# Kernel tuning notes

Hardware: AMD Instinct MI355X
Metric: run time of the kernel (lower is better)

The kernel has to match this reference:

```python
import jax, jax.numpy as jnp
import numpy as np

INPUT_DIM = 128
HIDDEN_DIM = 512
STACK_DIM = 64
BATCH = 128
MAX_T = 259  # 2*128 + 3
SEQ_L = 259  # l, so k = (l-3)//2 = 128


def setup_inputs() -> dict:
    key = jax.random.key(0)
    ks = jax.random.split(key, 7)
    G = 4 * HIDDEN_DIM
    x = jax.random.normal(ks[0], (SEQ_L, BATCH, INPUT_DIM), dtype=jnp.float32)
    Wih = jax.random.normal(ks[1], (G, INPUT_DIM + STACK_DIM), dtype=jnp.float32) * 0.05
    bih = jax.random.normal(ks[2], (G,), dtype=jnp.float32) * 0.05
    Whh = jax.random.normal(ks[3], (G, HIDDEN_DIM), dtype=jnp.float32) * 0.05
    bhh = jax.random.normal(ks[4], (G,), dtype=jnp.float32) * 0.05
    Wr = jax.random.normal(ks[5], (INPUT_DIM + STACK_DIM + 2, HIDDEN_DIM), dtype=jnp.float32) * 0.05
    br = jax.random.normal(ks[6], (INPUT_DIM + STACK_DIM + 2,), dtype=jnp.float32) * 0.05
    return {"x": x, "Wih": Wih, "bih": bih, "Whh": Whh, "bhh": bhh, "Wr": Wr, "br": br}


def _forward(x, Wih, bih, Whh, bhh, Wr, br):
    l = x.shape[0]
    k = (l - 3) // 2
    B = x.shape[1]

    def lstm_cell(xin, h, c):
        # torch.nn.LSTMCell: gate order i, f, g, o
        g = xin @ Wih.T + bih + h @ Whh.T + bhh  # [B, 4H]
        i, f, gg, o = jnp.split(g, 4, axis=1)
        c2 = jax.nn.sigmoid(f) * c + jax.nn.sigmoid(i) * jnp.tanh(gg)
        h2 = jax.nn.sigmoid(o) * jnp.tanh(c2)
        return h2, c2

    def update_stack(V, s, vt, ut, dt, t):
        Vp = V.at[:, t, :].add(vt)  # scatter vt into row t (row was zero)
        # baddbmm with strict-upper-triangular ones matrix == suffix sum:
        # prod[b, i] = sum_{j > i} s[b, j]
        prod = jnp.cumsum(s[:, ::-1], axis=1)[:, ::-1] - s
        sp = jnp.maximum(0.0, s - jnp.maximum(0.0, ut - prod))
        sp = sp.at[:, t].set(dt[:, 0])
        inner = jax.nn.relu(1.0 - prod - sp)  # uses prod from OLD s, as in source
        A = jnp.minimum(sp, inner)  # [B, MAX_T]
        rt = jnp.einsum('bt,btd->bd', A, Vp)
        return Vp, sp, rt

    def step(carry, inp):
        V, s, h, c, rt = carry
        xt, t = inp
        h, c = lstm_cell(jnp.concatenate([xt, rt], axis=1), h, c)
        out = h @ Wr.T + br  # [B, S + I + 2]
        vt = out[:, :STACK_DIM]
        ot = out[:, STACK_DIM:STACK_DIM + INPUT_DIM]
        ut = jax.nn.sigmoid(out[:, STACK_DIM + INPUT_DIM:STACK_DIM + INPUT_DIM + 1])
        dt = jax.nn.sigmoid(out[:, STACK_DIM + INPUT_DIM + 1:])
        V, s, rt = update_stack(V, s, vt, ut, dt, t)
        return (V, s, h, c, rt), ot

    dt_ = x.dtype
    carry = (jnp.zeros((B, MAX_T, STACK_DIM), dt_),
             jnp.zeros((B, MAX_T), dt_),
             jnp.zeros((B, HIDDEN_DIM), dt_),
             jnp.zeros((B, HIDDEN_DIM), dt_),
             jnp.zeros((B, STACK_DIM), dt_))
    # encode phase: steps 0..k with real inputs (outputs discarded)
    carry, _ = jax.lax.scan(step, carry, (x[:k + 1], jnp.arange(k + 1)))
    # decode phase: steps k+1..2k+2 with zero inputs (same encode_LSTM, per source)
    xz = jnp.zeros((k + 2, B, INPUT_DIM), dt_)
    carry, ots = jax.lax.scan(step, carry, (xz, k + 1 + jnp.arange(k + 2)))
    return jax.nn.log_softmax(ots, axis=2)  # [k+2, B, INPUT_DIM]


def reference(x, Wih, bih, Whh, bhh, Wr, br):
    return _forward(x, Wih, bih, Whh, bhh, Wr, br)
```

## Files before the change

kernel.cpp:

```cpp
#include <hip/hip_runtime.h>
#include <hip/hip_bf16.h>
#include <math.h>

#define IDIM 128
#define HDIM 512
#define SDIM 64
#define BATCH 128
#define MAXT 259
#define G4 2048
#define KTOT 704
#define ROUT 194
#define AFRAG_U 73728
#define NBLK 256
#define NGATE 16
#define PTJ 224
#define PCJ 80
#define POJ 128

typedef __hip_bfloat16 bf16;
typedef __attribute__((ext_vector_type(8))) short short8;
typedef __attribute__((ext_vector_type(4))) float floatx4;

__device__ __forceinline__ float sigmoidf_(float v) { return 1.f / (1.f + expf(-v)); }
__device__ __forceinline__ float b2f(bf16 v) { return __bfloat162float(v); }
__device__ __forceinline__ float load_in(const void* p, size_t i, int isf32) {
    return isf32 ? ((const float*)p)[i] : b2f(((const bf16*)p)[i]);
}
__device__ __forceinline__ unsigned short f2bfbits(float v) {
    unsigned u = __builtin_bit_cast(unsigned, v);
    unsigned r = (u + 0x7FFFu + ((u >> 16) & 1u)) >> 16;
    return (unsigned short)r;
}
__device__ __forceinline__ float bfbits2f(unsigned short b) {
    return __builtin_bit_cast(float, (unsigned)b << 16);
}
__device__ __forceinline__ unsigned aload(const unsigned* p) {
    return __hip_atomic_load(p, __ATOMIC_RELAXED, __HIP_MEMORY_SCOPE_AGENT);
}
__device__ __forceinline__ unsigned long long aload64(const unsigned long long* p) {
    return __hip_atomic_load(p, __ATOMIC_RELAXED, __HIP_MEMORY_SCOPE_AGENT);
}
__device__ __forceinline__ void astore32(unsigned* p, unsigned v) {
    __hip_atomic_store(p, v, __ATOMIC_RELAXED, __HIP_MEMORY_SCOPE_AGENT);
}
__device__ __forceinline__ void astore64(unsigned long long* p, unsigned long long v) {
    __hip_atomic_store(p, v, __ATOMIC_RELAXED, __HIP_MEMORY_SCOPE_AGENT);
}
__device__ __forceinline__ unsigned long long packf2(float a, float b) {
    return (unsigned long long)__builtin_bit_cast(unsigned, a)
         | ((unsigned long long)__builtin_bit_cast(unsigned, b) << 32);
}
__device__ __forceinline__ void unpack_frag(const unsigned long long* ap,
                                            short8& ah, short8& al) {
    #pragma unroll
    for (int j = 0; j < 4; j++) {
        unsigned long long q = aload64(ap + j);
        unsigned u0 = (unsigned)q, u1 = (unsigned)(q >> 32);
        ah[2 * j]     = (short)(u0 & 0xffffu);
        al[2 * j]     = (short)(u0 >> 16);
        ah[2 * j + 1] = (short)(u1 & 0xffffu);
        al[2 * j + 1] = (short)(u1 >> 16);
    }
}

__device__ __forceinline__ void wait_flags16(const unsigned* f, int base16,
                                             unsigned tgt) {
    if (threadIdx.x < 16) {
        while (aload(&f[(base16 + (int)threadIdx.x) * 16]) < tgt)
            __builtin_amdgcn_s_sleep(1);
    }
    __atomic_signal_fence(__ATOMIC_SEQ_CST);
    __syncthreads();
}

__global__ void detect_kernel(const unsigned short* __restrict__ w, int* __restrict__ flag) {
    if (threadIdx.x == 0) {
        int isf32 = 0;
        for (int i = 0; i < 256; i++) {
            int e = (w[i] >> 7) & 0xFF;
            if (e >= 0x8F) isf32 = 1;
        }
        *flag = isf32;
    }
}

__global__ void prep_kernel(const void* __restrict__ Wih, const void* __restrict__ bih,
                            const void* __restrict__ Whh, const void* __restrict__ bhh,
                            unsigned short* __restrict__ WfH, unsigned short* __restrict__ WfL,
                            float* __restrict__ bc, const int* __restrict__ flag) {
    int isf32 = *flag;
    int jp = blockIdx.x;
    int u = jp >> 2, gate = jp & 3;
    int src = gate * HDIM + u;
    int jt = jp >> 4, jn = jp & 15;
    for (int k = threadIdx.x; k < KTOT; k += blockDim.x) {
        float v = (k < 192) ? load_in(Wih, (size_t)src * 192 + k, isf32)
                            : load_in(Whh, (size_t)src * HDIM + (k - 192), isf32);
        unsigned short hi = f2bfbits(v);
        unsigned short lo = f2bfbits(v - bfbits2f(hi));
        int ks = k >> 5, q = (k & 31) >> 3, e = k & 7;
        size_t d = (((size_t)jt * 22 + ks) * 64 + (q * 16 + jn)) * 8 + e;
        WfH[d] = hi;
        WfL[d] = lo;
    }
    if (threadIdx.x == 0)
        bc[jp] = load_in(bih, src, isf32) + load_in(bhh, src, isf32);
}

__global__ void wr_prep_kernel(const void* __restrict__ Wr, const void* __restrict__ br,
                               unsigned short* __restrict__ WrBh, unsigned short* __restrict__ WrBl,
                               float* __restrict__ brf, const int* __restrict__ flag) {
    int isf32 = *flag;
    int j = blockIdx.x;
    for (int k = threadIdx.x; k < HDIM; k += blockDim.x) {
        float v = (j < ROUT) ? load_in(Wr, (size_t)j * HDIM + k, isf32) : 0.f;
        unsigned short hi = f2bfbits(v);
        WrBh[(size_t)j * HDIM + k] = hi;
        WrBl[(size_t)j * HDIM + k] = f2bfbits(v - bfbits2f(hi));
    }
    if (threadIdx.x == 0) brf[j] = (j < ROUT) ? load_in(br, j, isf32) : 0.f;
}

__global__ __launch_bounds__(256) void persist_kernel(
        const void* __restrict__ x,
        const unsigned short* __restrict__ WfH, const unsigned short* __restrict__ WfL,
        const float* __restrict__ bc,
        const unsigned short* __restrict__ WrBh, const unsigned short* __restrict__ WrBl,
        const float* __restrict__ brf,
        unsigned* __restrict__ AfP,
        float* __restrict__ partC,
        float* __restrict__ partO,
        unsigned short* __restrict__ Vg,
        void* __restrict__ dout, const int* __restrict__ flag,
        unsigned* __restrict__ hfl, unsigned* __restrict__ pfl,
        unsigned* __restrict__ rtf, unsigned* __restrict__ oflg) {
    __shared__ __align__(16) short Ahs[18 * 64 * 8];
    __shared__ __align__(16) short Als[18 * 64 * 8];
    __shared__ __align__(16) unsigned short wrslB[14 * 64 * 8];
    __shared__ __align__(16) unsigned short wrslBL[14 * 64 * 8];
    __shared__ __align__(16) float scr[8][16][20];
    __shared__ __align__(16) unsigned short hlh[16 * 40];
    __shared__ __align__(16) unsigned short hll[16 * 40];
    __shared__ __align__(16) float outsC[80];
    __shared__ __align__(16) float sL[324];
    __shared__ __align__(16) float aL[324];
    __shared__ __align__(16) float red[4][64];
    __shared__ __align__(16) float redo[128][2];
    __shared__ __align__(16) float oL[128];
    __shared__ __align__(16) float brS[208];
    __shared__ __align__(16) float bcS[128];
    __shared__ int e0S;

    const int tid = threadIdx.x, lane = tid & 63, wv = tid >> 6;
    const int blk = blockIdx.x, ms = blk >> 5, ns = blk & 31;
    const int isf32 = *flag;
    float* const pt = (float*)Ahs;

    const int is_gate = (ns < 16);
    const int gb = ns;
    const int pb = ns - 16;
    const int p2row = ms * 16 + pb;

    if (is_gate) {
        for (int i = tid; i < 14 * 64 * 8; i += 256) {
            int jt = i >> 9, l = (i >> 3) & 63, e = i & 7;
            size_t src = (size_t)(jt * 16 + (l & 15)) * HDIM + gb * 32 + (l >> 4) * 8 + e;
            wrslB[i]  = WrBh[src];
            wrslBL[i] = WrBl[src];
        }
        if (tid < 128) bcS[tid] = bc[gb * 128 + tid];
    } else {
        for (int i = tid; i < 208; i += 256) brS[i] = brf[i];
        for (int i = tid; i < 324; i += 256) { sL[i] = 0.f; aL[i] = 0.f; }
    }
    __syncthreads();

    if (is_gate) {
        const short8* WH = (const short8*)WfH;
        const short8* WL = (const short8*)WfL;
        const int jt0 = gb * 8 + wv, jt1 = gb * 8 + 4 + wv;
        const short8* wb0  = WH + (size_t)jt0 * 22 * 64;
        const short8* wb1  = WH + (size_t)jt1 * 22 * 64;
        const short8* wbl0 = WL + (size_t)jt0 * 22 * 64;
        const short8* wbl1 = WL + (size_t)jt1 * 22 * 64;
        float cc0 = 0.f, cc1 = 0.f;

        for (int t = 0; t < MAXT; t++) {
            const int cur = t & 1, nxt = cur ^ 1;
            const unsigned long long* AfPc64 =
                (const unsigned long long*)(AfP + (size_t)cur * AFRAG_U);
            unsigned long long* AfPn64 =
                (unsigned long long*)(AfP + (size_t)nxt * AFRAG_U);
            const int use_x = (t < 129);

            floatx4 acc0 = {0.f, 0.f, 0.f, 0.f};
            floatx4 acc1 = {0.f, 0.f, 0.f, 0.f};
            if (use_x) {
                int m = lane & 15, q = lane >> 4;
                size_t xrow = ((size_t)t * BATCH + ms * 16 + m) * IDIM + q * 8;
                #pragma unroll
                for (int ks = 0; ks < 4; ks++) {
                    short8 a;
                    if (isf32) {
                        const float* xf = (const float*)x + xrow + ks * 32;
                        #pragma unroll
                        for (int i = 0; i < 8; i++) a[i] = (short)f2bfbits(xf[i]);
                    } else {
                        a = *(const short8*)((const unsigned short*)x + xrow + ks * 32);
                    }
                    acc0 = __builtin_amdgcn_mfma_f32_16x16x32_bf16(a, wb0[ks * 64 + lane], acc0, 0, 0, 0);
                    acc1 = __builtin_amdgcn_mfma_f32_16x16x32_bf16(a, wb1[ks * 64 + lane], acc1, 0, 0, 0);
                    if (isf32) {
                        acc0 = __builtin_amdgcn_mfma_f32_16x16x32_bf16(a, wbl0[ks * 64 + lane], acc0, 0, 0, 0);
                        acc1 = __builtin_amdgcn_mfma_f32_16x16x32_bf16(a, wbl1[ks * 64 + lane], acc1, 0, 0, 0);
                    }
                }
            }

            wait_flags16(hfl, ms * 16, (unsigned)t);
            #pragma unroll
            for (int i0 = 0; i0 < 4; i0++) {
                int i = i0 * 256 + tid;
                int ksi = 2 + (i >> 6), l = i & 63;
                const unsigned long long* ap =
                    AfPc64 + ((size_t)(ms * 18 + ksi) * 64 + l) * 4;
                short8 ah, al8;
                unpack_frag(ap, ah, al8);
                *(short8*)&Ahs[(ksi * 64 + l) * 8] = ah;
                *(short8*)&Als[(ksi * 64 + l) * 8] = al8;
            }
            __syncthreads();

            #pragma unroll 4
            for (int ksi = 2; ksi < 18; ksi++) {
                int ks = 4 + ksi;
                short8 ah  = *(const short8*)&Ahs[(ksi * 64 + lane) * 8];
                short8 al8 = *(const short8*)&Als[(ksi * 64 + lane) * 8];
                short8 bh0 = wb0[ks * 64 + lane];
                short8 bh1 = wb1[ks * 64 + lane];
                acc0 = __builtin_amdgcn_mfma_f32_16x16x32_bf16(ah, bh0, acc0, 0, 0, 0);
                acc0 = __builtin_amdgcn_mfma_f32_16x16x32_bf16(al8, bh0, acc0, 0, 0, 0);
                acc1 = __builtin_amdgcn_mfma_f32_16x16x32_bf16(ah, bh1, acc1, 0, 0, 0);
                acc1 = __builtin_amdgcn_mfma_f32_16x16x32_bf16(al8, bh1, acc1, 0, 0, 0);
                if (isf32) {
                    acc0 = __builtin_amdgcn_mfma_f32_16x16x32_bf16(ah, wbl0[ks * 64 + lane], acc0, 0, 0, 0);
                    acc1 = __builtin_amdgcn_mfma_f32_16x16x32_bf16(ah, wbl1[ks * 64 + lane], acc1, 0, 0, 0);
                }
            }

            wait_flags16(rtf, ms * 16, (unsigned)t);
            if (tid < 128) {
                int ksi = tid >> 6, l = tid & 63;
                const unsigned long long* ap =
                    AfPc64 + ((size_t)(ms * 18 + ksi) * 64 + l) * 4;
                short8 ah, al8;
                unpack_frag(ap, ah, al8);
                *(short8*)&Ahs[(ksi * 64 + l) * 8] = ah;
                *(short8*)&Als[(ksi * 64 + l) * 8] = al8;
            }
            __syncthreads();
            #pragma unroll
            for (int ksi = 0; ksi < 2; ksi++) {
                int ks = 4 + ksi;
                short8 ah  = *(const short8*)&Ahs[(ksi * 64 + lane) * 8];
                short8 al8 = *(const short8*)&Als[(ksi * 64 + lane) * 8];
                short8 bh0 = wb0[ks * 64 + lane];
                short8 bh1 = wb1[ks * 64 + lane];
                acc0 = __builtin_amdgcn_mfma_f32_16x16x32_bf16(ah, bh0, acc0, 0, 0, 0);
                acc0 = __builtin_amdgcn_mfma_f32_16x16x32_bf16(al8, bh0, acc0, 0, 0, 0);
                acc1 = __builtin_amdgcn_mfma_f32_16x16x32_bf16(ah, bh1, acc1, 0, 0, 0);
                acc1 = __builtin_amdgcn_mfma_f32_16x16x32_bf16(al8, bh1, acc1, 0, 0, 0);
                if (isf32) {
                    acc0 = __builtin_amdgcn_mfma_f32_16x16x32_bf16(ah, wbl0[ks * 64 + lane], acc0, 0, 0, 0);
                    acc1 = __builtin_amdgcn_mfma_f32_16x16x32_bf16(ah, wbl1[ks * 64 + lane], acc1, 0, 0, 0);
                }
            }
            {
                int n = lane & 15, m0 = (lane >> 4) * 4;
                #pragma unroll
                for (int r = 0; r < 4; r++) scr[wv][m0 + r][n] = acc0[r];
                #pragma unroll
                for (int r = 0; r < 4; r++) scr[wv + 4][m0 + r][n] = acc1[r];
            }
            __syncthreads();
            {
                int r = tid >> 4, p = tid & 15;
                float4 g = *(const float4*)&scr[p >> 2][r][(p & 3) * 4];
                float4 bb = *(const float4*)&bcS[p * 4];
                float c2 = sigmoidf_(g.y + bb.y) * cc0 + sigmoidf_(g.x + bb.x) * tanhf(g.z + bb.z);
                float h2 = sigmoidf_(g.w + bb.w) * tanhf(c2);
                cc0 = c2;
                unsigned short hi0 = f2bfbits(h2);
                unsigned short lo0 = f2bfbits(h2 - bfbits2f(hi0));
                hlh[r * 40 + p] = hi0;
                hll[r * 40 + p] = lo0;
                int u1 = p + 16;
                float4 g1 = *(const float4*)&scr[u1 >> 2][r][(u1 & 3) * 4];
                float4 bb1 = *(const float4*)&bcS[u1 * 4];
                float c21 = sigmoidf_(g1.y + bb1.y) * cc1 + sigmoidf_(g1.x + bb1.x) * tanhf(g1.z + bb1.z);
                float h21 = sigmoidf_(g1.w + bb1.w) * tanhf(c21);
                cc1 = c21;
                unsigned short hi1 = f2bfbits(h21);
                unsigned short lo1 = f2bfbits(h21 - bfbits2f(hi1));
                hlh[r * 40 + u1] = hi1;
                hll[r * 40 + u1] = lo1;
                unsigned* AfPn32 = (unsigned*)AfPn64;
                size_t fb = ((size_t)ms * 18 + 2 + gb) * 64;
                size_t fi1 = (fb + (size_t)((p >> 3) * 16 + r)) * 8 + (p & 7);
                size_t fi2 = (fb + (size_t)((2 + (p >> 3)) * 16 + r)) * 8 + (p & 7);
                astore32(AfPn32 + fi1, (unsigned)hi0 | ((unsigned)lo0 << 16));
                astore32(AfPn32 + fi2, (unsigned)hi1 | ((unsigned)lo1 << 16));
            }
            asm volatile("s_waitcnt vmcnt(0)" ::: "memory");
            __syncthreads();
            if (tid == 0)
                __hip_atomic_store(&hfl[(ms * 16 + gb) * 16], (unsigned)(t + 1),
                                   __ATOMIC_RELAXED, __HIP_MEMORY_SCOPE_AGENT);

            {
                int m = lane & 15, q = lane >> 4;
                short8 ahh = *(const short8*)&hlh[m * 40 + q * 8];
                short8 ahl = *(const short8*)&hll[m * 40 + q * 8];
                int n = lane & 15, m0 = (lane >> 4) * 4;
                {
                    const short8* bB  = (const short8*)&wrslB[((size_t)wv * 64 + lane) * 8];
                    const short8* bBl = (const short8*)&wrslBL[((size_t)wv * 64 + lane) * 8];
                    floatx4 accR = {0.f, 0.f, 0.f, 0.f};
                    short8 bh = *bB;
                    accR = __builtin_amdgcn_mfma_f32_16x16x32_bf16(ahh, bh, accR, 0, 0, 0);
                    accR = __builtin_amdgcn_mfma_f32_16x16x32_bf16(ahl, bh, accR, 0, 0, 0);
                    if (isf32) {
                        short8 bl = *bBl;
                        accR = __builtin_amdgcn_mfma_f32_16x16x32_bf16(ahh, bl, accR, 0, 0, 0);
                        accR = __builtin_amdgcn_mfma_f32_16x16x32_bf16(ahl, bl, accR, 0, 0, 0);
                    }
                    #pragma unroll
                    for (int r = 0; r < 4; r++) {
                        int row = ms * 16 + m0 + r;
                        astore32((unsigned*)partC + ((size_t)row * NGATE + gb) * PCJ
                                     + wv * 16 + n,
                                 __builtin_bit_cast(unsigned, accR[r]));
                    }
                }
                if (wv == 0) {
                    const short8* bB  = (const short8*)&wrslB[((size_t)12 * 64 + lane) * 8];
                    const short8* bBl = (const short8*)&wrslBL[((size_t)12 * 64 + lane) * 8];
                    floatx4 accR = {0.f, 0.f, 0.f, 0.f};
                    short8 bh = *bB;
                    accR = __builtin_amdgcn_mfma_f32_16x16x32_bf16(ahh, bh, accR, 0, 0, 0);
                    accR = __builtin_amdgcn_mfma_f32_16x16x32_bf16(ahl, bh, accR, 0, 0, 0);
                    if (isf32) {
                        short8 bl = *bBl;
                        accR = __builtin_amdgcn_mfma_f32_16x16x32_bf16(ahh, bl, accR, 0, 0, 0);
                        accR = __builtin_amdgcn_mfma_f32_16x16x32_bf16(ahl, bl, accR, 0, 0, 0);
                    }
                    if (n < 2) {
                        #pragma unroll
                        for (int r = 0; r < 4; r++) {
                            int row = ms * 16 + m0 + r;
                            astore32((unsigned*)partC + ((size_t)row * NGATE + gb) * PCJ
                                         + 64 + n,
                                     __builtin_bit_cast(unsigned, accR[r]));
                        }
                    }
                }
            }
            asm volatile("s_waitcnt vmcnt(0)" ::: "memory");
            __syncthreads();
            if (tid == 0)
                __hip_atomic_store(&pfl[(ms * 16 + gb) * 16], (unsigned)(t + 1),
                                   __ATOMIC_RELAXED, __HIP_MEMORY_SCOPE_AGENT);

            if (!use_x) {
                {
                    int m = lane & 15, q = lane >> 4;
                    short8 ahh = *(const short8*)&hlh[m * 40 + q * 8];
                    short8 ahl = *(const short8*)&hll[m * 40 + q * 8];
                    int n = lane & 15, m0 = (lane >> 4) * 4;
                    #pragma unroll
                    for (int s2 = 0; s2 < 2; s2++) {
                        int jt = 4 + wv + s2 * 4;
                        const short8* bB  = (const short8*)&wrslB[((size_t)jt * 64 + lane) * 8];
                        const short8* bBl = (const short8*)&wrslBL[((size_t)jt * 64 + lane) * 8];
                        floatx4 accR = {0.f, 0.f, 0.f, 0.f};
                        short8 bh = *bB;
                        accR = __builtin_amdgcn_mfma_f32_16x16x32_bf16(ahh, bh, accR, 0, 0, 0);
                        accR = __builtin_amdgcn_mfma_f32_16x16x32_bf16(ahl, bh, accR, 0, 0, 0);
                        if (isf32) {
                            short8 bl = *bBl;
                            accR = __builtin_amdgcn_mfma_f32_16x16x32_bf16(ahh, bl, accR, 0, 0, 0);
                            accR = __builtin_amdgcn_mfma_f32_16x16x32_bf16(ahl, bl, accR, 0, 0, 0);
                        }
                        #pragma unroll
                        for (int ri = 0; ri < 4; ri++)
                            pt[(m0 + ri) * PTJ + jt * 16 + n] = accR[ri];
                    }
                }
                __syncthreads();
                {
                    #pragma unroll
                    for (int it = 0; it < 4; it++) {
                        int rloc = wv * 4 + it;
                        int prow_ = ms * 16 + rloc;
                        const float* pr = pt + rloc * PTJ;
                        unsigned long long* pb64 = (unsigned long long*)
                            (partO + ((((size_t)cur * BATCH + prow_) * NGATE) + gb) * POJ);
                        astore64(pb64 + lane, packf2(pr[64 + 2 * lane], pr[65 + 2 * lane]));
                    }
                }
                asm volatile("s_waitcnt vmcnt(0)" ::: "memory");
                __syncthreads();
                if (tid == 0)
                    __hip_atomic_store(&oflg[(ms * 16 + gb) * 16], (unsigned)(t + 1),
                                       __ATOMIC_RELAXED, __HIP_MEMORY_SCOPE_AGENT);
            }
        }
    } else {
        unsigned short* Vrow = Vg + (size_t)p2row * MAXT * SDIM;
        for (int t = 0; t < MAXT; t++) {
            unsigned long long* AfPn64 =
                (unsigned long long*)(AfP + (size_t)((t + 1) & 1) * AFRAG_U);

            wait_flags16(pfl, ms * 16, (unsigned)(t + 1));

            if (tid < 66) {
                const unsigned* pb2 = (const unsigned*)partC
                                    + (size_t)p2row * NGATE * PCJ + tid;
                float s4 = (tid < 64) ? brS[tid] : brS[128 + tid];
                #pragma unroll
                for (int g = 0; g < NGATE; g++)
                    s4 += __builtin_bit_cast(float, aload(pb2 + (size_t)g * PCJ));
                outsC[tid] = s4;
            }
            __syncthreads();
            if (wv == 0) {
                float uval = sigmoidf_(outsC[64]);
                float dval = sigmoidf_(outsC[65]);
                Vrow[t * SDIM + lane] = f2bfbits(outsC[lane]);
                int ebase = lane * 5;
                float sv[5], suf[5];
                #pragma unroll
                for (int j = 0; j < 5; j++) {
                    int e = ebase + j;
                    sv[j] = (e < MAXT) ? sL[e] : 0.f;
                }
                suf[4] = sv[4];
                #pragma unroll
                for (int j = 3; j >= 0; j--) suf[j] = sv[j] + suf[j + 1];
                float ltot = suf[0];
                float accs = ltot;
                #pragma unroll
                for (int off = 1; off < 64; off <<= 1) {
                    float y = __shfl_down(accs, off, 64);
                    if (lane + off < 64) accs += y;
                }
                float after_lane = accs - ltot;
                int emin = 0x7fffffff;
                #pragma unroll
                for (int j = 0; j < 5; j++) {
                    int e = ebase + j;
                    if (e <= t) {
                        float prod = after_lane + (suf[j] - sv[j]);
                        float sp = (e == t) ? dval
                                            : fmaxf(0.f, sv[j] - fmaxf(0.f, uval - prod));
                        float inner = fmaxf(0.f, 1.f - prod - sp);
                        sL[e] = sp;
                        aL[e] = fminf(sp, inner);
                        if (prod < 1.f && e < emin) emin = e;
                    }
                }
                #pragma unroll
                for (int off = 32; off; off >>= 1) {
                    int o = __shfl_xor(emin, off, 64);
                    emin = o < emin ? o : emin;
                }
                if (lane == 0) e0S = emin;
            }
            __syncthreads();
            {
                const int e0 = e0S;
                float racc = 0.f;
                if (e0 <= t) {
                    int i2s = e0 + ((wv - e0) & 3);
                    for (int i2 = i2s; i2 <= t; i2 += 4)
                        racc += aL[i2] * bfbits2f(Vrow[i2 * SDIM + lane]);
                }
                red[wv][lane] = racc;
            }
            __syncthreads();
            if (wv == 0) {
                float rtv = red[0][lane] + red[1][lane] + red[2][lane] + red[3][lane];
                float rtn = __shfl_down(rtv, 1, 64);
                if ((lane & 1) == 0) {
                    unsigned short hb0 = f2bfbits(rtv);
                    unsigned short lb0 = f2bfbits(rtv - bfbits2f(hb0));
                    unsigned short hb1 = f2bfbits(rtn);
                    unsigned short lb1 = f2bfbits(rtn - bfbits2f(hb1));
                    unsigned u0 = (unsigned)hb0 | ((unsigned)lb0 << 16);
                    unsigned u1 = (unsigned)hb1 | ((unsigned)lb1 << 16);
                    int d0 = lane;
                    int ksi = d0 >> 5, q = (d0 & 31) >> 3, e = d0 & 7;
                    size_t fi = (((size_t)ms * 18 + ksi) * 64 + q * 16 + pb) * 8 + e;
                    astore64(AfPn64 + fi / 2,
                             (unsigned long long)u0 | ((unsigned long long)u1 << 32));
                }
                asm volatile("s_waitcnt vmcnt(0)" ::: "memory");
                if (lane == 0)
                    __hip_atomic_store(&rtf[(ms * 16 + pb) * 16], (unsigned)(t + 1),
                                       __ATOMIC_RELAXED, __HIP_MEMORY_SCOPE_AGENT);
            }
            if (t >= 129) {
                wait_flags16(oflg, ms * 16, (unsigned)(t + 1));
                {
                    int col = tid >> 1, half = tid & 1;
                    const unsigned* pbo = (const unsigned*)partO
                        + (((size_t)(t & 1) * BATCH + p2row) * NGATE) * POJ + col;
                    float s = 0.f;
                    #pragma unroll
                    for (int g = 0; g < 8; g++)
                        s += __builtin_bit_cast(float,
                                aload(pbo + (size_t)(half * 8 + g) * POJ));
                    redo[col][half] = s;
                }
                __syncthreads();
                if (tid < 128) oL[tid] = redo[tid][0] + redo[tid][1] + brS[64 + tid];
                __syncthreads();
                if (wv == 0) {
                    float a = oL[lane];
                    float bvv = oL[64 + lane];
                    float m = fmaxf(a, bvv);
                    #pragma unroll
                    for (int off = 32; off; off >>= 1) m = fmaxf(m, __shfl_xor(m, off, 64));
                    float e = expf(a - m) + expf(bvv - m);
                    #pragma unroll
                    for (int off = 32; off; off >>= 1) e += __shfl_xor(e, off, 64);
                    float ls = logf(e) + m;
                    size_t base = ((size_t)(t - 129) * BATCH + p2row) * IDIM;
                    if (isf32) {
                        ((float*)dout)[base + lane] = a - ls;
                        ((float*)dout)[base + lane + 64] = bvv - ls;
                    } else {
                        ((bf16*)dout)[base + lane] = __float2bfloat16(a - ls);
                        ((bf16*)dout)[base + lane + 64] = __float2bfloat16(bvv - ls);
                    }
                }
            }
        }
    }
}

extern "C" void kernel_launch(void* const* d_in, const int* in_sizes, int n_in,
                              void* d_out, int out_size, void* d_ws, size_t ws_size,
                              hipStream_t stream) {
    const void* x   = d_in[0];
    const void* Wih = d_in[1];
    const void* bih = d_in[2];
    const void* Whh = d_in[3];
    const void* bhh = d_in[4];
    const void* Wr  = d_in[5];
    const void* br  = d_in[6];

    char* base = (char*)d_ws;
    size_t off = 0;
    int* flag = (int*)base;                                   off += 64;
    unsigned* hfl = (unsigned*)(base + off);                  off += 128 * 64 + 64;
    unsigned* pfl = (unsigned*)(base + off);                  off += 128 * 64 + 64;
    unsigned* rtf = (unsigned*)(base + off);                  off += 128 * 64 + 64;
    unsigned* oflg = (unsigned*)(base + off);                 off += 128 * 64 + 64;
    unsigned short* WfH  = (unsigned short*)(base + off);     off += (size_t)G4 * KTOT * 2;
    unsigned short* WfL  = (unsigned short*)(base + off);     off += (size_t)G4 * KTOT * 2;
    unsigned short* WrBh = (unsigned short*)(base + off);     off += (size_t)224 * HDIM * 2;
    unsigned short* WrBl = (unsigned short*)(base + off);     off += (size_t)224 * HDIM * 2;
    float* bc   = (float*)(base + off);                       off += G4 * 4;
    float* brf  = (float*)(base + off);                       off += 1024;
    unsigned* AfP = (unsigned*)(base + off);                  size_t af_off = off;
                                                              off += (size_t)2 * AFRAG_U * 4;
    float* partC = (float*)(base + off);                      off += (size_t)BATCH * NGATE * PCJ * 4;
    float* partO = (float*)(base + off);                      off += (size_t)2 * BATCH * NGATE * POJ * 4;
    unsigned short* Vg = (unsigned short*)(base + off);       off += (size_t)BATCH * MAXT * SDIM * 2;

    hipMemsetAsync(base + 64, 0, 4 * (128 * 64 + 64), stream);
    hipMemsetAsync(base + af_off, 0, (size_t)2 * AFRAG_U * 4, stream);
    hipMemsetAsync(partC, 0, (size_t)BATCH * NGATE * PCJ * 4, stream);

    detect_kernel<<<1, 64, 0, stream>>>((const unsigned short*)Wih, flag);
    prep_kernel<<<G4, 256, 0, stream>>>(Wih, bih, Whh, bhh, WfH, WfL, bc, flag);
    wr_prep_kernel<<<224, 256, 0, stream>>>(Wr, br, WrBh, WrBl, brf, flag);

    persist_kernel<<<NBLK, 256, 0, stream>>>(x, WfH, WfL, bc, WrBh, WrBl, brf,
                                             AfP, partC, partO, Vg, d_out, flag,
                                             hfl, pfl, rtf, oflg);

    (void)in_sizes; (void)n_in; (void)out_size; (void)ws_size;
}
```

Measured before the change: 2.990 ms.

## Compute stack-control projection in stack blocks directly from h, dropping partC handoff

```diff
diff --git a/kernel.cpp b/kernel.cpp
--- a/kernel.cpp
+++ b/kernel.cpp
@@ -14,7 +14,6 @@
 #define NBLK 256
 #define NGATE 16
 #define PTJ 224
-#define PCJ 80
 #define POJ 128
 
 typedef __hip_bfloat16 bf16;
@@ -128,12 +127,11 @@
         const unsigned short* __restrict__ WrBh, const unsigned short* __restrict__ WrBl,
         const float* __restrict__ brf,
         unsigned* __restrict__ AfP,
-        float* __restrict__ partC,
         float* __restrict__ partO,
         unsigned short* __restrict__ Vg,
         void* __restrict__ dout, const int* __restrict__ flag,
-        unsigned* __restrict__ hfl, unsigned* __restrict__ pfl,
-        unsigned* __restrict__ rtf, unsigned* __restrict__ oflg) {
+        unsigned* __restrict__ hfl, unsigned* __restrict__ rtf,
+        unsigned* __restrict__ oflg) {
     __shared__ __align__(16) short Ahs[18 * 64 * 8];
     __shared__ __align__(16) short Als[18 * 64 * 8];
     __shared__ __align__(16) unsigned short wrslB[14 * 64 * 8];
@@ -141,10 +139,13 @@
     __shared__ __align__(16) float scr[8][16][20];
     __shared__ __align__(16) unsigned short hlh[16 * 40];
     __shared__ __align__(16) unsigned short hll[16 * 40];
+    __shared__ __align__(16) float hL[512];
     __shared__ __align__(16) float outsC[80];
     __shared__ __align__(16) float sL[324];
     __shared__ __align__(16) float aL[324];
     __shared__ __align__(16) float red[4][64];
+    __shared__ __align__(16) float redc[64][4];
+    __shared__ __align__(16) float redud[2][4];
     __shared__ __align__(16) float redo[128][2];
     __shared__ __align__(16) float oL[128];
     __shared__ __align__(16) float brS[208];
@@ -317,60 +318,6 @@
                 __hip_atomic_store(&hfl[(ms * 16 + gb) * 16], (unsigned)(t + 1),
                                    __ATOMIC_RELAXED, __HIP_MEMORY_SCOPE_AGENT);
 
-            {
-                int m = lane & 15, q = lane >> 4;
-                short8 ahh = *(const short8*)&hlh[m * 40 + q * 8];
-                short8 ahl = *(const short8*)&hll[m * 40 + q * 8];
-                int n = lane & 15, m0 = (lane >> 4) * 4;
-                {
-                    const short8* bB  = (const short8*)&wrslB[((size_t)wv * 64 + lane) * 8];
-                    const short8* bBl = (const short8*)&wrslBL[((size_t)wv * 64 + lane) * 8];
-                    floatx4 accR = {0.f, 0.f, 0.f, 0.f};
-                    short8 bh = *bB;
-                    accR = __builtin_amdgcn_mfma_f32_16x16x32_bf16(ahh, bh, accR, 0, 0, 0);
-                    accR = __builtin_amdgcn_mfma_f32_16x16x32_bf16(ahl, bh, accR, 0, 0, 0);
-                    if (isf32) {
-                        short8 bl = *bBl;
-                        accR = __builtin_amdgcn_mfma_f32_16x16x32_bf16(ahh, bl, accR, 0, 0, 0);
-                        accR = __builtin_amdgcn_mfma_f32_16x16x32_bf16(ahl, bl, accR, 0, 0, 0);
-                    }
-                    #pragma unroll
-                    for (int r = 0; r < 4; r++) {
-                        int row = ms * 16 + m0 + r;
-                        astore32((unsigned*)partC + ((size_t)row * NGATE + gb) * PCJ
-                                     + wv * 16 + n,
-                                 __builtin_bit_cast(unsigned, accR[r]));
-                    }
-                }
-                if (wv == 0) {
-                    const short8* bB  = (const short8*)&wrslB[((size_t)12 * 64 + lane) * 8];
-                    const short8* bBl = (const short8*)&wrslBL[((size_t)12 * 64 + lane) * 8];
-                    floatx4 accR = {0.f, 0.f, 0.f, 0.f};
-                    short8 bh = *bB;
-                    accR = __builtin_amdgcn_mfma_f32_16x16x32_bf16(ahh, bh, accR, 0, 0, 0);
-                    accR = __builtin_amdgcn_mfma_f32_16x16x32_bf16(ahl, bh, accR, 0, 0, 0);
-                    if (isf32) {
-                        short8 bl = *bBl;
-                        accR = __builtin_amdgcn_mfma_f32_16x16x32_bf16(ahh, bl, accR, 0, 0, 0);
-                        accR = __builtin_amdgcn_mfma_f32_16x16x32_bf16(ahl, bl, accR, 0, 0, 0);
-                    }
-                    if (n < 2) {
-                        #pragma unroll
-                        for (int r = 0; r < 4; r++) {
-                            int row = ms * 16 + m0 + r;
-                            astore32((unsigned*)partC + ((size_t)row * NGATE + gb) * PCJ
-                                         + 64 + n,
-                                     __builtin_bit_cast(unsigned, accR[r]));
-                        }
-                    }
-                }
-            }
-            asm volatile("s_waitcnt vmcnt(0)" ::: "memory");
-            __syncthreads();
-            if (tid == 0)
-                __hip_atomic_store(&pfl[(ms * 16 + gb) * 16], (unsigned)(t + 1),
-                                   __ATOMIC_RELAXED, __HIP_MEMORY_SCOPE_AGENT);
-
             if (!use_x) {
                 {
                     int m = lane & 15, q = lane >> 4;
@@ -418,20 +365,83 @@
     } else {
         unsigned short* Vrow = Vg + (size_t)p2row * MAXT * SDIM;
         for (int t = 0; t < MAXT; t++) {
+            const int pn = (t + 1) & 1;
+            const unsigned* Afn32 = (const unsigned*)(AfP + (size_t)pn * AFRAG_U);
             unsigned long long* AfPn64 =
-                (unsigned long long*)(AfP + (size_t)((t + 1) & 1) * AFRAG_U);
-
-            wait_flags16(pfl, ms * 16, (unsigned)(t + 1));
-
-            if (tid < 66) {
-                const unsigned* pb2 = (const unsigned*)partC
-                                    + (size_t)p2row * NGATE * PCJ + tid;
-                float s4 = (tid < 64) ? brS[tid] : brS[128 + tid];
-                #pragma unroll
-                for (int g = 0; g < NGATE; g++)
-                    s4 += __builtin_bit_cast(float, aload(pb2 + (size_t)g * PCJ));
-                outsC[tid] = s4;
-            }
+                (unsigned long long*)(AfP + (size_t)pn * AFRAG_U);
+
+            wait_flags16(hfl, ms * 16, (unsigned)(t + 1));
+
+            {
+                int u = 2 * tid;
+                size_t fi = (((size_t)ms * 18 + 2 + (u >> 5)) * 64
+                             + (size_t)(((u & 31) >> 3) * 16 + pb)) * 8 + (u & 7);
+                unsigned long long q = aload64((const unsigned long long*)Afn32 + fi / 2);
+                unsigned w0 = (unsigned)q, w1 = (unsigned)(q >> 32);
+                hL[u]     = bfbits2f((unsigned short)(w0 & 0xffffu))
+                          + bfbits2f((unsigned short)(w0 >> 16));
+                hL[u + 1] = bfbits2f((unsigned short)(w1 & 0xffffu))
+                          + bfbits2f((unsigned short)(w1 >> 16));
+            }
+            __syncthreads();
+            {
+                int j = tid >> 2, ks0 = (tid & 3) * 128;
+                const unsigned short* wr = WrBh + (size_t)j * HDIM + ks0;
+                float s = 0.f;
+                #pragma unroll 4
+                for (int k0 = 0; k0 < 128; k0 += 8) {
+                    short8 w = *(const short8*)(wr + k0);
+                    float4 hv0 = *(const float4*)&hL[ks0 + k0];
+                    float4 hv1 = *(const float4*)&hL[ks0 + k0 + 4];
+                    s += bfbits2f((unsigned short)w[0]) * hv0.x + bfbits2f((unsigned short)w[1]) * hv0.y
+                       + bfbits2f((unsigned short)w[2]) * hv0.z + bfbits2f((unsigned short)w[3]) * hv0.w
+                       + bfbits2f((unsigned short)w[4]) * hv1.x + bfbits2f((unsigned short)w[5]) * hv1.y
+                       + bfbits2f((unsigned short)w[6]) * hv1.z + bfbits2f((unsigned short)w[7]) * hv1.w;
+                }
+                if (isf32) {
+                    const unsigned short* wrl = WrBl + (size_t)j * HDIM + ks0;
+                    #pragma unroll 4
+                    for (int k0 = 0; k0 < 128; k0 += 8) {
+                        short8 w = *(const short8*)(wrl + k0);
+                        float4 hv0 = *(const float4*)&hL[ks0 + k0];
+                        float4 hv1 = *(const float4*)&hL[ks0 + k0 + 4];
+                        s += bfbits2f((unsigned short)w[0]) * hv0.x + bfbits2f((unsigned short)w[1]) * hv0.y
+                           + bfbits2f((unsigned short)w[2]) * hv0.z + bfbits2f((unsigned short)w[3]) * hv0.w
+                           + bfbits2f((unsigned short)w[4]) * hv1.x + bfbits2f((unsigned short)w[5]) * hv1.y
+                           + bfbits2f((unsigned short)w[6]) * hv1.z + bfbits2f((unsigned short)w[7]) * hv1.w;
+                    }
+                }
+                redc[j][tid & 3] = s;
+                if (tid < 8) {
+                    int j2 = 192 + (tid >> 2), k2 = (tid & 3) * 128;
+                    const unsigned short* wr2 = WrBh + (size_t)j2 * HDIM + k2;
+                    float s2 = 0.f;
+                    #pragma unroll 4
+                    for (int k0 = 0; k0 < 128; k0 += 8) {
+                        short8 w = *(const short8*)(wr2 + k0);
+                        #pragma unroll
+                        for (int e = 0; e < 8; e++)
+                            s2 += bfbits2f((unsigned short)w[e]) * hL[k2 + k0 + e];
+                    }
+                    if (isf32) {
+                        const unsigned short* wrl2 = WrBl + (size_t)j2 * HDIM + k2;
+                        #pragma unroll 4
+                        for (int k0 = 0; k0 < 128; k0 += 8) {
+                            short8 w = *(const short8*)(wrl2 + k0);
+                            #pragma unroll
+                            for (int e = 0; e < 8; e++)
+                                s2 += bfbits2f((unsigned short)w[e]) * hL[k2 + k0 + e];
+                        }
+                    }
+                    redud[tid >> 2][tid & 3] = s2;
+                }
+            }
+            __syncthreads();
+            if (tid < 64)
+                outsC[tid] = redc[tid][0] + redc[tid][1] + redc[tid][2] + redc[tid][3] + brS[tid];
+            else if (tid < 66)
+                outsC[tid] = redud[tid - 64][0] + redud[tid - 64][1]
+                           + redud[tid - 64][2] + redud[tid - 64][3] + brS[128 + tid];
             __syncthreads();
             if (wv == 0) {
                 float uval = sigmoidf_(outsC[64]);
@@ -564,7 +574,6 @@
     size_t off = 0;
     int* flag = (int*)base;                                   off += 64;
     unsigned* hfl = (unsigned*)(base + off);                  off += 128 * 64 + 64;
-    unsigned* pfl = (unsigned*)(base + off);                  off += 128 * 64 + 64;
     unsigned* rtf = (unsigned*)(base + off);                  off += 128 * 64 + 64;
     unsigned* oflg = (unsigned*)(base + off);                 off += 128 * 64 + 64;
     unsigned short* WfH  = (unsigned short*)(base + off);     off += (size_t)G4 * KTOT * 2;
@@ -575,21 +584,19 @@
     float* brf  = (float*)(base + off);                       off += 1024;
     unsigned* AfP = (unsigned*)(base + off);                  size_t af_off = off;
                                                               off += (size_t)2 * AFRAG_U * 4;
-    float* partC = (float*)(base + off);                      off += (size_t)BATCH * NGATE * PCJ * 4;
     float* partO = (float*)(base + off);                      off += (size_t)2 * BATCH * NGATE * POJ * 4;
     unsigned short* Vg = (unsigned short*)(base + off);       off += (size_t)BATCH * MAXT * SDIM * 2;
 
-    hipMemsetAsync(base + 64, 0, 4 * (128 * 64 + 64), stream);
+    hipMemsetAsync(base + 64, 0, 3 * (128 * 64 + 64), stream);
     hipMemsetAsync(base + af_off, 0, (size_t)2 * AFRAG_U * 4, stream);
-    hipMemsetAsync(partC, 0, (size_t)BATCH * NGATE * PCJ * 4, stream);
 
     detect_kernel<<<1, 64, 0, stream>>>((const unsigned short*)Wih, flag);
     prep_kernel<<<G4, 256, 0, stream>>>(Wih, bih, Whh, bhh, WfH, WfL, bc, flag);
     wr_prep_kernel<<<224, 256, 0, stream>>>(Wr, br, WrBh, WrBl, brf, flag);
 
     persist_kernel<<<NBLK, 256, 0, stream>>>(x, WfH, WfL, bc, WrBh, WrBl, brf,
-                                             AfP, partC, partO, Vg, d_out, flag,
-                                             hfl, pfl, rtf, oflg);
+                                             AfP, partO, Vg, d_out, flag,
+                                             hfl, rtf, oflg);
 
     (void)in_sizes; (void)n_in; (void)out_size; (void)ws_size;
 }
```

Result: slower. 3.511 ms (+17.4%).
